# Optimization experiments

Measured on AMD Instinct MI355X. Metric: run time of the kernel, lower is better.

## Reference

```python
import jax, jax.numpy as jnp
from jax import lax
import numpy as np

H, W = 512, 1024
PAD = 7            # (kernel_size*2)//2 used for the 1x1 box-conv padding
POOL = 7           # max-pool NMS window
TOP_K = 200
NC = 34            # num semantic classes
B = 2
Hp, Wp = H + 2 * PAD, W + 2 * PAD


def _xy():
    # matches registered xy_coords buffer: (x,y) grids, 1-based
    xg = jnp.tile(jnp.arange(1, W + 1, dtype=jnp.float32)[None, :], (H, 1))
    yg = jnp.tile(jnp.arange(1, H + 1, dtype=jnp.float32)[:, None], (1, W))
    return jnp.stack([xg, yg], 0)  # [2,H,W]


def setup_inputs():
    key = jax.random.key(0)
    k1, k2 = jax.random.split(key)
    segmentation_probs = jax.random.normal(k1, (B, NC, H, W), jnp.float32)
    xy = _xy()
    blk = 64.0
    sx = jnp.floor((xy[0] - 1.0) / blk) * blk + blk / 2.0
    sy = jnp.floor((xy[1] - 1.0) / blk) * blk + blk / 2.0
    snapped = jnp.stack([sx, sy], 0)  # per-pixel block-center vote target
    noise = 0.05 * jax.random.normal(k2, (B, 2, H, W), jnp.float32)
    center_regressions = xy[None] - snapped[None] + noise
    center_maps_placeholder = jnp.zeros((1,), jnp.float32)
    return {"segmentation_probs": segmentation_probs,
            "center_maps_placeholder": center_maps_placeholder,
            "center_regressions": center_regressions}


def _assign(ccp, centers, valid):
    # ccp [B,2,H,W] predicted (x,y) centers per pixel; centers [B,K,2] as (y,x)
    # in padded coords (replicates original frame mismatch); valid [B,K].
    # Streaming argmin over K centers: O(B*H*W) memory.
    Bn = ccp.shape[0]
    def step(carry, k):
        bd, bi = carry
        cy = centers[:, k, 0].astype(jnp.float32)[:, None, None]
        cx = centers[:, k, 1].astype(jnp.float32)[:, None, None]
        d = (ccp[:, 0] - cx) ** 2 + (ccp[:, 1] - cy) ** 2  # sqrt omitted: argmin-invariant
        d = jnp.where(valid[:, k][:, None, None], d, jnp.inf)
        upd = d < bd
        return (jnp.where(upd, d, bd), jnp.where(upd, k, bi)), None
    init = (jnp.full((Bn, H, W), jnp.inf, jnp.float32),
            jnp.full((Bn, H, W), -1, jnp.int32))
    (bd, bi), _ = lax.scan(step, init, jnp.arange(TOP_K, dtype=jnp.int32))
    return bi + 1  # label 0 <=> no valid center


def _seg_sum(v, lab):
    return jax.ops.segment_sum(v.ravel(), lab.ravel(), num_segments=TOP_K + 1)

def _seg_min(v, lab):
    return jax.ops.segment_min(v.ravel(), lab.ravel(), num_segments=TOP_K + 1)

def _seg_max(v, lab):
    return jax.ops.segment_max(v.ravel(), lab.ravel(), num_segments=TOP_K + 1)


def _forward(segmentation_probs, center_regressions):
    seg_probs = jax.nn.softmax(segmentation_probs, axis=1)          # [B,NC,H,W]
    seg_map = jnp.argmax(segmentation_probs, axis=1).astype(jnp.float32)  # [B,H,W]
    xy = _xy()
    ccp = xy[None] - center_regressions                             # [B,2,H,W]
    # Threshold(23.99,50) then <=33  <=>  class in (23.99, 33]
    things = (seg_map > 23.99) & (seg_map <= 33.0)

    # ---- vote scatter (unique+counts == scatter-add of ones) ----
    vx = jnp.round(ccp[:, 0]).astype(jnp.int32)
    vy = jnp.round(ccp[:, 1]).astype(jnp.int32)
    ok = things & (vx >= 0) & (vy >= 0) & (vx < W) & (vy < H)
    flat = jnp.where(ok, vy * W + vx, H * W)                        # invalid -> dummy bin
    vote = jax.vmap(lambda ix: jnp.zeros(H * W + 1, jnp.float32).at[ix.ravel()].add(1.0))(flat)
    vote = vote[:, : H * W].reshape(-1, H, W)

    # ---- 1x1 box conv with padding=7 (just zero-pads), maxpool NMS ----
    aggr = jnp.pad(vote, ((0, 0), (PAD, PAD), (PAD, PAD)))          # [B,Hp,Wp]
    pooled = lax.reduce_window(aggr, -jnp.inf, lax.max, (1, POOL, POOL), (1, 1, 1),
                               [(0, 0), (POOL // 2, POOL // 2), (POOL // 2, POOL // 2)])
    nms = jnp.where(pooled == aggr, aggr, 0.0)
    cm = jnp.where(nms > 50.0, nms, 0.0)                            # Threshold(50,0)

    # ---- top-k centers by vote count ----
    vals = jnp.where(cm > 0.0, aggr, -1.0).reshape(-1, Hp * Wp)
    tv, ti = lax.top_k(vals, TOP_K)
    coords = jnp.stack([ti // Wp, ti % Wp], -1)                     # [B,K,2] (y,x)
    cvalid = tv > 0.0
    any_c = cvalid.any(-1)
    thingsi = things.astype(jnp.int32)

    lab0 = _assign(ccp, coords, cvalid) * thingsi
    lab0 = jnp.where(any_c[:, None, None], lab0, 0)

    ones_hw = jnp.ones((H, W), jnp.float32)
    ygrid = jnp.tile(jnp.arange(H, dtype=jnp.float32)[:, None], (1, W))
    xgrid = jnp.tile(jnp.arange(W, dtype=jnp.float32)[None, :], (H, 1))

    # ---- b_box_ratio_pruning2 ----
    cnt = jax.vmap(_seg_sum, (None, 0))(ones_hw, lab0)              # [B,K+1]
    ymin = jax.vmap(_seg_min, (None, 0))(ygrid, lab0)
    ymax = jax.vmap(_seg_max, (None, 0))(ygrid, lab0)
    xmin = jax.vmap(_seg_min, (None, 0))(xgrid, lab0)
    xmax = jax.vmap(_seg_max, (None, 0))(xgrid, lab0)
    ratio = cnt / ((ymax - ymin + 1.0) * (xmax - xmin + 1.0))
    g1 = ((cnt > 0) & (ratio > 0.3))[:, 1:]                         # [B,K] good slots
    n1 = g1.sum(-1)
    lab1s = _assign(ccp, coords, g1) * thingsi
    nl1 = jnp.cumsum(g1.astype(jnp.int32), -1)                      # compact relabel 1..n1
    lab1 = jax.vmap(lambda nl, l: jnp.where(l > 0, nl[l - 1], 0))(nl1, lab1s)
    lab1 = jnp.where((n1 > 0)[:, None, None], lab1, lab0)

    # ---- remove_high_mean_centers (indexes ORIGINAL sorted coords, as in source) ----
    cnt2 = jax.vmap(_seg_sum, (None, 0))(ones_hw, lab1)
    sx = jax.vmap(_seg_sum)(center_regressions[:, 0], lab1)
    sy = jax.vmap(_seg_sum)(center_regressions[:, 1], lab1)
    mx = sx / jnp.maximum(cnt2, 1.0)
    my = sy / jnp.maximum(cnt2, 1.0)
    g2 = ((cnt2 > 0) & (jnp.abs(mx) < 10.0) & (jnp.abs(my) < 10.0))[:, 1:]
    n2 = g2.sum(-1)
    lab2s = _assign(ccp, coords, g2) * thingsi
    nl2 = jnp.cumsum(g2.astype(jnp.int32), -1)
    lab2 = jax.vmap(lambda nl, l: jnp.where(l > 0, nl[l - 1], 0))(nl2, lab2s)
    final = jnp.where((n2 > 0)[:, None, None], lab2, lab1)

    # ---- separate_inst_maps: per-instance class (mode), mean class prob, size ----
    segc = seg_map.astype(jnp.int32)
    hidx = final * NC + segc
    hist = jax.vmap(lambda ix: jax.ops.segment_sum(
        jnp.ones(H * W, jnp.float32), ix.ravel(), num_segments=(TOP_K + 1) * NC))(hidx)
    hist = hist.reshape(-1, TOP_K + 1, NC)
    inst_class = jnp.argmax(hist, -1)                               # [B,K+1]
    # S[b,c,j] = sum of seg_probs[b,c] over pixels of instance j
    S = jax.vmap(lambda p, l: jax.vmap(lambda pc: _seg_sum(pc, l))(p))(seg_probs, final)
    cntf = jax.vmap(_seg_sum, (None, 0))(ones_hw, final)
    Sg = jnp.take_along_axis(jnp.swapaxes(S, 1, 2), inst_class[..., None], -1)[..., 0]
    seg_prob = Sg / jnp.maximum(cntf, 1.0)                          # [B,K+1]
    return final, seg_map, inst_class, seg_prob, cntf


def reference(segmentation_probs, center_maps_placeholder, center_regressions):
    return _forward(segmentation_probs, center_regressions)
```

## Files before the change

### kernel.cpp

```cpp
#include <hip/hip_runtime.h>
#include <stdint.h>

#define HH   512
#define WW   1024
#define BB   2
#define NCC  34
#define PADK 7
#define TOPK 200
#define NSEG (TOPK + 1)
#define WPAD (WW + 2 * PADK)
#define NPIX (HH * WW)
#define CAP  12288
#define INTMAXC  0x7FFFFFFF
#define INTMINC  (-0x7FFFFFFF - 1)

struct Prm {
  const float* seg; const float* cr;
  float* out_final; float* out_segmap; float* out_instc; float* out_prob; float* out_cntf;
  int32_t* labA; int32_t* labB; float* mbuf; float* invs; uint8_t* segc;
  int* ymin; int* ymax; int* xmin; int* xmax; int* instc;
  uint4* zero4; int nzero4;
  uint32_t* cand_cnt; uint32_t* cand_val; uint32_t* cand_idx;
  float* slotx; float* sloty; int* n0;
  float* l1x; float* l1y; int* n1;
  float* l2x; float* l2y; int* n2;
  uint32_t* cnt0; uint32_t* cnt2; long long* sxq; long long* syq;
  uint32_t* hist; long long* Ssel;
};

__global__ __launch_bounds__(256) void k_clear(Prm p) {
  int t = blockIdx.x * 256 + threadIdx.x;
  if (t < BB * NPIX / 4) reinterpret_cast<uint4*>(p.labA)[t] = make_uint4(0u, 0u, 0u, 0u);
  if (t < p.nzero4) p.zero4[t] = make_uint4(0u, 0u, 0u, 0u);
  if (t < BB * NSEG) {
    p.ymin[t] = INTMAXC; p.ymax[t] = INTMINC; p.xmin[t] = INTMAXC; p.xmax[t] = INTMINC;
  }
}

__global__ __launch_bounds__(256) void k_pixel(Prm p) {
  int t = blockIdx.x * 256 + threadIdx.x;
  int b = t >> 17;
  int pp = (t & 131071) << 2;
  int h = pp >> 10, w = pp & 1023;
  size_t i = (size_t)b * NPIX + pp;
  const float* base = p.seg + (size_t)b * NCC * NPIX + pp;
  float4 m = *reinterpret_cast<const float4*>(base);
  float4 s = make_float4(__expf(m.x), __expf(m.y), __expf(m.z), __expf(m.w));
  int4 am = make_int4(0, 0, 0, 0);
  #pragma unroll
  for (int c = 1; c < NCC; ++c) {
    float4 x = *reinterpret_cast<const float4*>(base + (size_t)c * NPIX);
    s.x += __expf(x.x); if (x.x > m.x) { m.x = x.x; am.x = c; }
    s.y += __expf(x.y); if (x.y > m.y) { m.y = x.y; am.y = c; }
    s.z += __expf(x.z); if (x.z > m.z) { m.z = x.z; am.z = c; }
    s.w += __expf(x.w); if (x.w > m.w) { m.w = x.w; am.w = c; }
  }
  *reinterpret_cast<float4*>(p.out_segmap + i) =
      make_float4((float)am.x, (float)am.y, (float)am.z, (float)am.w);
  *reinterpret_cast<uchar4*>(p.segc + i) =
      make_uchar4((unsigned char)am.x, (unsigned char)am.y, (unsigned char)am.z, (unsigned char)am.w);
  *reinterpret_cast<float4*>(p.mbuf + i) = m;
  *reinterpret_cast<float4*>(p.invs + i) =
      make_float4(__expf(m.x) / s.x, __expf(m.y) / s.y, __expf(m.z) / s.z, __expf(m.w) / s.w);

  const float* c0 = p.cr + (size_t)b * 2 * NPIX + pp;
  float4 r0 = *reinterpret_cast<const float4*>(c0);
  float4 r1 = *reinterpret_cast<const float4*>(c0 + NPIX);
  float crx[4] = {r0.x, r0.y, r0.z, r0.w};
  float cry[4] = {r1.x, r1.y, r1.z, r1.w};
  int amA[4] = {am.x, am.y, am.z, am.w};
  int tgt[4];
  #pragma unroll
  for (int q = 0; q < 4; ++q) {
    tgt[q] = -1;
    if (amA[q] >= 24) {
      float ccx = (float)(w + q + 1) - crx[q];
      float ccy = (float)(h + 1) - cry[q];
      float rx = rintf(ccx), ry = rintf(ccy);
      if (rx >= 0.f && ry >= 0.f && rx < (float)WW && ry < (float)HH)
        tgt[q] = (int)ry * WW + (int)rx;
    }
  }
  int lane = threadIdx.x & 63;
  uint32_t* vb = (uint32_t*)p.labA + (size_t)b * NPIX;
  #pragma unroll
  for (int q = 0; q < 4; ++q) {
    int tq = tgt[q];
    unsigned long long act = __ballot(tq >= 0);
    while (act) {
      int leader = __ffsll(act) - 1;
      int tl = __shfl(tq, leader);
      unsigned long long mt = __ballot(tq == tl);
      if (lane == leader) atomicAdd(&vb[tl], (uint32_t)__popcll(mt & act));
      act &= ~mt;
    }
  }
}

__global__ __launch_bounds__(256) void k_nms(Prm p) {
  int t = blockIdx.x * 256 + threadIdx.x;
  int b = t >> 17;
  int pp = (t & 131071) << 2;
  int h = pp >> 10, w0 = pp & 1023;
  const uint32_t* vb = (const uint32_t*)p.labA + (size_t)b * NPIX;
  uint4 v4 = *reinterpret_cast<const uint4*>(vb + pp);
  uint32_t vv[4] = {v4.x, v4.y, v4.z, v4.w};
  #pragma unroll
  for (int q = 0; q < 4; ++q) {
    uint32_t v = vv[q];
    if (v <= 50u) continue;
    int w = w0 + q;
    bool peak = true;
    for (int dy = -3; dy <= 3 && peak; ++dy) {
      int yy = h + dy; if (yy < 0 || yy >= HH) continue;
      for (int dx = -3; dx <= 3; ++dx) {
        int xx = w + dx; if (xx < 0 || xx >= WW) continue;
        if (vb[yy * WW + xx] > v) { peak = false; break; }
      }
    }
    if (!peak) continue;
    uint32_t pos = atomicAdd(&p.cand_cnt[b], 1u);
    if (pos < CAP) {
      p.cand_val[b * CAP + pos] = v;
      p.cand_idx[b * CAP + pos] = (uint32_t)((h + PADK) * WPAD + (w + PADK));
    }
  }
}

__global__ void k_topk(Prm p) {
  int b = blockIdx.x;
  int n = (int)p.cand_cnt[b]; if (n > CAP) n = CAP;
  const uint32_t* cv = p.cand_val + b * CAP;
  const uint32_t* ci = p.cand_idx + b * CAP;
  for (int i = threadIdx.x; i < n; i += blockDim.x) {
    unsigned long long ki = ((unsigned long long)cv[i] << 20) | (unsigned long long)(0xFFFFFu - ci[i]);
    int r = 0;
    for (int j = 0; j < n; ++j) {
      unsigned long long kj = ((unsigned long long)cv[j] << 20) | (unsigned long long)(0xFFFFFu - ci[j]);
      r += (kj > ki) ? 1 : 0;
    }
    if (r < TOPK) {
      uint32_t idx = ci[i];
      p.slotx[b * TOPK + r] = (float)(idx % WPAD);
      p.sloty[b * TOPK + r] = (float)(idx / WPAD);
    }
  }
  if (threadIdx.x == 0) p.n0[b] = (n < TOPK) ? n : TOPK;
}

__device__ __forceinline__ int prune_centers(int n, const float* __restrict__ sxs,
    const float* __restrict__ sys, float minx, float maxx, float miny, float maxy,
    short* __restrict__ clist, int lane) {
  #pragma unroll
  for (int o = 32; o; o >>= 1) {
    minx = fminf(minx, __shfl_xor(minx, o));
    maxx = fmaxf(maxx, __shfl_xor(maxx, o));
    miny = fminf(miny, __shfl_xor(miny, o));
    maxy = fmaxf(maxy, __shfl_xor(maxy, o));
  }
  float cx0 = 0.5f * (minx + maxx), rx = 0.5f * (maxx - minx) + 0.5f;
  float cy0 = 0.5f * (miny + maxy), ry = 0.5f * (maxy - miny) + 0.5f;
  float lo[4];
  float ub = 3.4e38f;
  #pragma unroll
  for (int c = 0; c < 4; ++c) {
    int k = c * 64 + lane;
    float l = 3.4e38f;
    if (k < n) {
      float dx = fabsf(sxs[k] - cx0), dy = fabsf(sys[k] - cy0);
      float hx = dx + rx, hy = dy + ry;
      ub = fminf(ub, hx * hx + hy * hy);
      float lx = fmaxf(dx - rx, 0.f), ly = fmaxf(dy - ry, 0.f);
      l = lx * lx + ly * ly;
    }
    lo[c] = l;
  }
  #pragma unroll
  for (int o = 32; o; o >>= 1) ub = fminf(ub, __shfl_xor(ub, o));
  ub += 1.0f;
  int m = 0;
  unsigned long long lmlt = (1ull << lane) - 1ull;
  #pragma unroll
  for (int c = 0; c < 4; ++c) {
    int k = c * 64 + lane;
    bool keep = (k < n) && (lo[c] <= ub);
    unsigned long long msk = __ballot(keep);
    if (keep) clist[m + (int)__popcll(msk & lmlt)] = (short)k;
    m += (int)__popcll(msk);
  }
  return m;
}

__device__ __forceinline__ void assign4_exact(int m, const short* __restrict__ clist,
    const float* __restrict__ sxs, const float* __restrict__ sys,
    const float* ccx, const float* ccy, const unsigned char* cls, int* l) {
  float bd[4] = {3.4e38f, 3.4e38f, 3.4e38f, 3.4e38f};
  int bk[4] = {0, 0, 0, 0};
  for (int j = 0; j < m; ++j) {
    int k = (int)clist[j];
    float cxk = sxs[k], cyk = sys[k];
    #pragma unroll
    for (int q = 0; q < 4; ++q) {
      float dx = ccx[q] - cxk, dy = ccy[q] - cyk;
      float d = __fadd_rn(__fmul_rn(dx, dx), __fmul_rn(dy, dy));
      if (d < bd[q]) { bd[q] = d; bk[q] = k; }
    }
  }
  #pragma unroll
  for (int q = 0; q < 4; ++q) l[q] = (cls[q] >= 24) ? bk[q] + 1 : 0;
}

__global__ __launch_bounds__(256) void k_assign0(Prm p) {
  int b = blockIdx.y, h = blockIdx.x;
  __shared__ float sxs[TOPK], sys[TOPK];
  __shared__ short clists[4][TOPK];
  __shared__ uint32_t sc[NSEG];
  __shared__ int sx0[NSEG], sx1[NSEG];
  int n = p.n0[b];
  for (int k = threadIdx.x; k < n; k += 256) { sxs[k] = p.slotx[b * TOPK + k]; sys[k] = p.sloty[b * TOPK + k]; }
  for (int j = threadIdx.x; j < NSEG; j += 256) { sc[j] = 0; sx0[j] = INTMAXC; sx1[j] = INTMINC; }
  __syncthreads();
  int w = threadIdx.x * 4;
  size_t i = (size_t)b * NPIX + h * WW + w;
  const float* c0 = p.cr + (size_t)b * 2 * NPIX + h * WW + w;
  uchar4 sc4 = *reinterpret_cast<const uchar4*>(p.segc + i);
  float4 r0 = *reinterpret_cast<const float4*>(c0);
  float4 r1 = *reinterpret_cast<const float4*>(c0 + NPIX);
  int l[4];
  if (n == 0) { l[0] = l[1] = l[2] = l[3] = 0; }
  else {
    float ccx[4], ccy[4];
    #pragma unroll
    for (int q = 0; q < 4; ++q) {
      ccx[q] = (float)(w + q + 1) - ((const float*)&r0)[q];
      ccy[q] = (float)(h + 1) - ((const float*)&r1)[q];
    }
    float mnx = fminf(fminf(ccx[0], ccx[1]), fminf(ccx[2], ccx[3]));
    float mxx = fmaxf(fmaxf(ccx[0], ccx[1]), fmaxf(ccx[2], ccx[3]));
    float mny = fminf(fminf(ccy[0], ccy[1]), fminf(ccy[2], ccy[3]));
    float mxy = fmaxf(fmaxf(ccy[0], ccy[1]), fmaxf(ccy[2], ccy[3]));
    int lane = threadIdx.x & 63, wv = threadIdx.x >> 6;
    int m = prune_centers(n, sxs, sys, mnx, mxx, mny, mxy, clists[wv], lane);
    unsigned char cls[4] = {sc4.x, sc4.y, sc4.z, sc4.w};
    assign4_exact(m, clists[wv], sxs, sys, ccx, ccy, cls, l);
  }
  *reinterpret_cast<int4*>(p.labA + i) = make_int4(l[0], l[1], l[2], l[3]);
  int cur = -1; uint32_t rc = 0; int rx0 = 0, rx1 = 0;
  #pragma unroll
  for (int q = 0; q < 4; ++q) {
    int lq = l[q], x = w + q;
    if (lq == cur) { rc++; rx1 = x; }
    else {
      if (cur > 0) { atomicAdd(&sc[cur], rc); atomicMin(&sx0[cur], rx0); atomicMax(&sx1[cur], rx1); }
      cur = lq; rc = 1; rx0 = rx1 = x;
    }
  }
  if (cur > 0) { atomicAdd(&sc[cur], rc); atomicMin(&sx0[cur], rx0); atomicMax(&sx1[cur], rx1); }
  __syncthreads();
  for (int j = threadIdx.x; j < NSEG; j += 256) {
    if (sc[j]) {
      atomicAdd(&p.cnt0[b * NSEG + j], sc[j]);
      atomicMin(&p.ymin[b * NSEG + j], h); atomicMax(&p.ymax[b * NSEG + j], h);
      atomicMin(&p.xmin[b * NSEG + j], sx0[j]); atomicMax(&p.xmax[b * NSEG + j], sx1[j]);
    }
  }
}

__global__ void k_build1(Prm p) {
  int b = blockIdx.x;
  __shared__ int good[TOPK], pref[TOPK];
  int k = threadIdx.x;
  if (k < TOPK) {
    uint32_t c = p.cnt0[b * NSEG + k + 1];
    int g = 0;
    if (c > 0) {
      int j = b * NSEG + k + 1;
      float area = (float)((p.ymax[j] - p.ymin[j] + 1) * (p.xmax[j] - p.xmin[j] + 1));
      float ratio = (float)c / area;
      g = (ratio > 0.3f) ? 1 : 0;
    }
    good[k] = g;
  }
  __syncthreads();
  if (threadIdx.x == 0) {
    int s = 0;
    for (int j = 0; j < TOPK; ++j) { pref[j] = s; s += good[j]; }
    p.n1[b] = s;
  }
  __syncthreads();
  if (k < TOPK && good[k]) {
    int r = pref[k];
    p.l1x[b * TOPK + r] = p.slotx[b * TOPK + k];
    p.l1y[b * TOPK + r] = p.sloty[b * TOPK + k];
  }
}

__global__ __launch_bounds__(256) void k_assign1(Prm p) {
  int b = blockIdx.y, h = blockIdx.x;
  __shared__ float sxs[TOPK], sys[TOPK];
  __shared__ short clists[4][TOPK];
  __shared__ uint32_t sc[NSEG];
  __shared__ unsigned long long ssx[NSEG], ssy[NSEG];
  int n = p.n1[b];
  for (int k = threadIdx.x; k < n; k += 256) { sxs[k] = p.l1x[b * TOPK + k]; sys[k] = p.l1y[b * TOPK + k]; }
  for (int j = threadIdx.x; j < NSEG; j += 256) { sc[j] = 0; ssx[j] = 0; ssy[j] = 0; }
  __syncthreads();
  int w = threadIdx.x * 4;
  size_t i = (size_t)b * NPIX + h * WW + w;
  const float* c0 = p.cr + (size_t)b * 2 * NPIX + h * WW + w;
  uchar4 sc4 = *reinterpret_cast<const uchar4*>(p.segc + i);
  float4 r0 = *reinterpret_cast<const float4*>(c0);
  float4 r1 = *reinterpret_cast<const float4*>(c0 + NPIX);
  int l[4];
  if (n == 0) { int4 f = *reinterpret_cast<const int4*>(p.labA + i); l[0]=f.x; l[1]=f.y; l[2]=f.z; l[3]=f.w; }
  else {
    float ccx[4], ccy[4];
    #pragma unroll
    for (int q = 0; q < 4; ++q) {
      ccx[q] = (float)(w + q + 1) - ((const float*)&r0)[q];
      ccy[q] = (float)(h + 1) - ((const float*)&r1)[q];
    }
    float mnx = fminf(fminf(ccx[0], ccx[1]), fminf(ccx[2], ccx[3]));
    float mxx = fmaxf(fmaxf(ccx[0], ccx[1]), fmaxf(ccx[2], ccx[3]));
    float mny = fminf(fminf(ccy[0], ccy[1]), fminf(ccy[2], ccy[3]));
    float mxy = fmaxf(fmaxf(ccy[0], ccy[1]), fmaxf(ccy[2], ccy[3]));
    int lane = threadIdx.x & 63, wv = threadIdx.x >> 6;
    int m = prune_centers(n, sxs, sys, mnx, mxx, mny, mxy, clists[wv], lane);
    unsigned char cls[4] = {sc4.x, sc4.y, sc4.z, sc4.w};
    assign4_exact(m, clists[wv], sxs, sys, ccx, ccy, cls, l);
  }
  *reinterpret_cast<int4*>(p.labB + i) = make_int4(l[0], l[1], l[2], l[3]);
  float crx[4] = {r0.x, r0.y, r0.z, r0.w};
  float cry[4] = {r1.x, r1.y, r1.z, r1.w};
  int cur = -1; uint32_t rc = 0; long long ax = 0, ay = 0;
  #pragma unroll
  for (int q = 0; q < 4; ++q) {
    int lq = l[q];
    long long qx = __double2ll_rn((double)crx[q] * 1048576.0);
    long long qy = __double2ll_rn((double)cry[q] * 1048576.0);
    if (lq == cur) { rc++; ax += qx; ay += qy; }
    else {
      if (cur > 0) { atomicAdd(&sc[cur], rc);
                     atomicAdd(&ssx[cur], (unsigned long long)ax);
                     atomicAdd(&ssy[cur], (unsigned long long)ay); }
      cur = lq; rc = 1; ax = qx; ay = qy;
    }
  }
  if (cur > 0) { atomicAdd(&sc[cur], rc);
                 atomicAdd(&ssx[cur], (unsigned long long)ax);
                 atomicAdd(&ssy[cur], (unsigned long long)ay); }
  __syncthreads();
  for (int j = threadIdx.x; j < NSEG; j += 256) {
    if (sc[j]) {
      atomicAdd(&p.cnt2[b * NSEG + j], sc[j]);
      atomicAdd((unsigned long long*)&p.sxq[b * NSEG + j], ssx[j]);
      atomicAdd((unsigned long long*)&p.syq[b * NSEG + j], ssy[j]);
    }
  }
}

__global__ void k_build2(Prm p) {
  int b = blockIdx.x;
  __shared__ int good[TOPK], pref[TOPK];
  int k = threadIdx.x;
  if (k < TOPK) {
    uint32_t c = p.cnt2[b * NSEG + k + 1];
    int g = 0;
    if (c > 0) {
      double inv = 1.0 / (double)c;
      double mx = ((double)p.sxq[b * NSEG + k + 1] * (1.0 / 1048576.0)) * inv;
      double my = ((double)p.syq[b * NSEG + k + 1] * (1.0 / 1048576.0)) * inv;
      g = (fabs(mx) < 10.0 && fabs(my) < 10.0) ? 1 : 0;
    }
    good[k] = g;
  }
  __syncthreads();
  if (threadIdx.x == 0) {
    int s = 0;
    for (int j = 0; j < TOPK; ++j) { pref[j] = s; s += good[j]; }
    p.n2[b] = s;
  }
  __syncthreads();
  if (k < TOPK && good[k]) {
    int r = pref[k];
    p.l2x[b * TOPK + r] = p.slotx[b * TOPK + k];
    p.l2y[b * TOPK + r] = p.sloty[b * TOPK + k];
  }
}

__global__ __launch_bounds__(256) void k_assign2(Prm p) {
  int b = blockIdx.y, h = blockIdx.x;
  __shared__ float sxs[TOPK], sys[TOPK];
  __shared__ short clists[4][TOPK];
  __shared__ uint32_t sh[NSEG * NCC];
  int n = p.n2[b];
  for (int k = threadIdx.x; k < n; k += 256) { sxs[k] = p.l2x[b * TOPK + k]; sys[k] = p.l2y[b * TOPK + k]; }
  for (int j = threadIdx.x; j < NSEG * NCC; j += 256) sh[j] = 0;
  __syncthreads();
  int w = threadIdx.x * 4;
  size_t i = (size_t)b * NPIX + h * WW + w;
  const float* c0 = p.cr + (size_t)b * 2 * NPIX + h * WW + w;
  uchar4 sc4 = *reinterpret_cast<const uchar4*>(p.segc + i);
  float4 r0 = *reinterpret_cast<const float4*>(c0);
  float4 r1 = *reinterpret_cast<const float4*>(c0 + NPIX);
  int l[4];
  if (n == 0) { int4 f = *reinterpret_cast<const int4*>(p.labB + i); l[0]=f.x; l[1]=f.y; l[2]=f.z; l[3]=f.w; }
  else {
    float ccx[4], ccy[4];
    #pragma unroll
    for (int q = 0; q < 4; ++q) {
      ccx[q] = (float)(w + q + 1) - ((const float*)&r0)[q];
      ccy[q] = (float)(h + 1) - ((const float*)&r1)[q];
    }
    float mnx = fminf(fminf(ccx[0], ccx[1]), fminf(ccx[2], ccx[3]));
    float mxx = fmaxf(fmaxf(ccx[0], ccx[1]), fmaxf(ccx[2], ccx[3]));
    float mny = fminf(fminf(ccy[0], ccy[1]), fminf(ccy[2], ccy[3]));
    float mxy = fmaxf(fmaxf(ccy[0], ccy[1]), fmaxf(ccy[2], ccy[3]));
    int lane = threadIdx.x & 63, wv = threadIdx.x >> 6;
    int m = prune_centers(n, sxs, sys, mnx, mxx, mny, mxy, clists[wv], lane);
    unsigned char cls[4] = {sc4.x, sc4.y, sc4.z, sc4.w};
    assign4_exact(m, clists[wv], sxs, sys, ccx, ccy, cls, l);
  }
  *reinterpret_cast<int4*>(p.labA + i) = make_int4(l[0], l[1], l[2], l[3]);
  *reinterpret_cast<float4*>(p.out_final + i) =
      make_float4((float)l[0], (float)l[1], (float)l[2], (float)l[3]);
  unsigned char cls[4] = {sc4.x, sc4.y, sc4.z, sc4.w};
  int curk = -1; uint32_t rc = 0;
  #pragma unroll
  for (int q = 0; q < 4; ++q) {
    int key = l[q] * NCC + (int)cls[q];
    if (key == curk) { rc++; }
    else { if (curk >= 0) atomicAdd(&sh[curk], rc); curk = key; rc = 1; }
  }
  if (curk >= 0) atomicAdd(&sh[curk], rc);
  __syncthreads();
  for (int j = threadIdx.x; j < NSEG * NCC; j += 256)
    if (sh[j]) atomicAdd(&p.hist[(size_t)b * NSEG * NCC + j], sh[j]);
}

__global__ void k_mode(Prm p) {
  int b = blockIdx.x;
  int j = threadIdx.x;
  if (j >= NSEG) return;
  const uint32_t* hr = p.hist + ((size_t)b * NSEG + j) * NCC;
  uint32_t bv = hr[0], s = hr[0]; int bc = 0;
  #pragma unroll
  for (int c = 1; c < NCC; ++c) {
    uint32_t v = hr[c]; s += v;
    if (v > bv) { bv = v; bc = c; }
  }
  p.instc[b * NSEG + j] = bc;
  p.out_instc[b * NSEG + j] = (float)bc;
  p.out_cntf[b * NSEG + j] = (float)s;
}

__global__ __launch_bounds__(256) void k_sg(Prm p) {
  int b = blockIdx.y;
  __shared__ unsigned long long ss[NSEG];
  __shared__ int icS[NSEG];
  for (int j = threadIdx.x; j < NSEG; j += 256) { ss[j] = 0; icS[j] = p.instc[b * NSEG + j]; }
  __syncthreads();
  int pp = (blockIdx.x * 256 + threadIdx.x) * 4;
  size_t i = (size_t)b * NPIX + pp;
  int4 l4 = *reinterpret_cast<const int4*>(p.labA + i);
  float4 mb = *reinterpret_cast<const float4*>(p.mbuf + i);
  float4 iv = *reinterpret_cast<const float4*>(p.invs + i);
  const float* sb = p.seg + (size_t)b * NCC * NPIX + pp;
  int lA[4] = {l4.x, l4.y, l4.z, l4.w};
  float mbA[4] = {mb.x, mb.y, mb.z, mb.w};
  float ivA[4] = {iv.x, iv.y, iv.z, iv.w};
  int cur = -1; long long acc = 0;
  #pragma unroll
  for (int q = 0; q < 4; ++q) {
    int lq = lA[q];
    int c = icS[lq];
    float x = sb[(size_t)c * NPIX + q];
    float pr = __expf(x - mbA[q]) * ivA[q];
    long long qv = __double2ll_rn((double)pr * 4294967296.0);
    if (lq == cur) acc += qv;
    else { if (cur >= 0) atomicAdd(&ss[cur], (unsigned long long)acc); cur = lq; acc = qv; }
  }
  if (cur >= 0) atomicAdd(&ss[cur], (unsigned long long)acc);
  __syncthreads();
  for (int j = threadIdx.x; j < NSEG; j += 256)
    if (ss[j]) atomicAdd((unsigned long long*)&p.Ssel[b * NSEG + j], ss[j]);
}

__global__ void k_prob(Prm p) {
  int i = blockIdx.x * blockDim.x + threadIdx.x;
  if (i >= BB * NSEG) return;
  double s = (double)p.Ssel[i] * (1.0 / 4294967296.0);
  float c = p.out_cntf[i];
  p.out_prob[i] = (float)(s / (double)fmaxf(c, 1.0f));
}

extern "C" void kernel_launch(void* const* d_in, const int* in_sizes, int n_in,
                              void* d_out, int out_size, void* d_ws, size_t ws_size,
                              hipStream_t stream) {
  float* out = (float*)d_out;
  Prm p;
  p.seg = (const float*)d_in[0];
  p.cr  = (const float*)d_in[2];
  p.out_final  = out;
  p.out_segmap = out + (size_t)BB * NPIX;
  p.out_instc  = out + (size_t)2 * BB * NPIX;
  p.out_prob   = p.out_instc + BB * NSEG;
  p.out_cntf   = p.out_prob + BB * NSEG;

  char* ws = (char*)d_ws;
  size_t off = 0;
  auto take = [&](size_t n) { size_t o = off; off += (n + 255) & ~(size_t)255; return o; };

  p.labA = (int32_t*)(ws + take((size_t)BB * NPIX * 4));
  p.labB = (int32_t*)(ws + take((size_t)BB * NPIX * 4));
  p.mbuf = (float*)(ws + take((size_t)BB * NPIX * 4));
  p.invs = (float*)(ws + take((size_t)BB * NPIX * 4));
  p.segc = (uint8_t*)(ws + take((size_t)BB * NPIX));
  p.ymin = (int*)(ws + take(BB * NSEG * 4));
  p.ymax = (int*)(ws + take(BB * NSEG * 4));
  p.xmin = (int*)(ws + take(BB * NSEG * 4));
  p.xmax = (int*)(ws + take(BB * NSEG * 4));

  size_t zero_begin = off;
  p.cand_cnt = (uint32_t*)(ws + take(BB * 4));
  p.cand_val = (uint32_t*)(ws + take((size_t)BB * CAP * 4));
  p.cand_idx = (uint32_t*)(ws + take((size_t)BB * CAP * 4));
  p.slotx = (float*)(ws + take(BB * TOPK * 4));
  p.sloty = (float*)(ws + take(BB * TOPK * 4));
  p.n0 = (int*)(ws + take(BB * 4));
  p.l1x = (float*)(ws + take(BB * TOPK * 4));
  p.l1y = (float*)(ws + take(BB * TOPK * 4));
  p.n1 = (int*)(ws + take(BB * 4));
  p.l2x = (float*)(ws + take(BB * TOPK * 4));
  p.l2y = (float*)(ws + take(BB * TOPK * 4));
  p.n2 = (int*)(ws + take(BB * 4));
  p.cnt0 = (uint32_t*)(ws + take(BB * NSEG * 4));
  p.cnt2 = (uint32_t*)(ws + take(BB * NSEG * 4));
  p.sxq = (long long*)(ws + take(BB * NSEG * 8));
  p.syq = (long long*)(ws + take(BB * NSEG * 8));
  p.hist = (uint32_t*)(ws + take((size_t)BB * NSEG * NCC * 4));
  p.instc = (int*)(ws + take(BB * NSEG * 4));
  p.Ssel = (long long*)(ws + take(BB * NSEG * 8));
  size_t zero_end = off;

  if (ws_size < off) return;

  p.zero4 = (uint4*)(ws + zero_begin);
  p.nzero4 = (int)((zero_end - zero_begin) / 16);

  k_clear<<<BB * NPIX / 4 / 256, 256, 0, stream>>>(p);
  k_pixel<<<BB * NPIX / 4 / 256, 256, 0, stream>>>(p);
  k_nms<<<BB * NPIX / 4 / 256, 256, 0, stream>>>(p);
  k_topk<<<BB, 256, 0, stream>>>(p);
  dim3 rgrid(HH, BB);
  k_assign0<<<rgrid, 256, 0, stream>>>(p);
  k_build1<<<BB, 256, 0, stream>>>(p);
  k_assign1<<<rgrid, 256, 0, stream>>>(p);
  k_build2<<<BB, 256, 0, stream>>>(p);
  k_assign2<<<rgrid, 256, 0, stream>>>(p);
  k_mode<<<BB, 256, 0, stream>>>(p);
  k_sg<<<dim3(NPIX / 1024, BB), 256, 0, stream>>>(p);
  k_prob<<<(BB * NSEG + 255) / 256, 256, 0, stream>>>(p);
}
```

Baseline: 134.2 us.

## Fuse top-k, build and mode kernels into per-row assign blocks

```diff
diff --git a/kernel.cpp b/kernel.cpp
--- a/kernel.cpp
+++ b/kernel.cpp
@@ -11,19 +11,17 @@
 #define WPAD (WW + 2 * PADK)
 #define NPIX (HH * WW)
 #define CAP  12288
+#define KSTG 1024
 #define INTMAXC  0x7FFFFFFF
 #define INTMINC  (-0x7FFFFFFF - 1)
 
 struct Prm {
   const float* seg; const float* cr;
   float* out_final; float* out_segmap; float* out_instc; float* out_prob; float* out_cntf;
-  int32_t* labA; int32_t* labB; float* mbuf; float* invs; uint8_t* segc;
-  int* ymin; int* ymax; int* xmin; int* xmax; int* instc;
+  int32_t* labA; int32_t* labB; float* pinv; uint8_t* segc;
+  int* ymin; int* ymax; int* xmin; int* xmax;
   uint4* zero4; int nzero4;
   uint32_t* cand_cnt; uint32_t* cand_val; uint32_t* cand_idx;
-  float* slotx; float* sloty; int* n0;
-  float* l1x; float* l1y; int* n1;
-  float* l2x; float* l2y; int* n2;
   uint32_t* cnt0; uint32_t* cnt2; long long* sxq; long long* syq;
   uint32_t* hist; long long* Ssel;
 };
@@ -59,9 +57,8 @@
       make_float4((float)am.x, (float)am.y, (float)am.z, (float)am.w);
   *reinterpret_cast<uchar4*>(p.segc + i) =
       make_uchar4((unsigned char)am.x, (unsigned char)am.y, (unsigned char)am.z, (unsigned char)am.w);
-  *reinterpret_cast<float4*>(p.mbuf + i) = m;
-  *reinterpret_cast<float4*>(p.invs + i) =
-      make_float4(__expf(m.x) / s.x, __expf(m.y) / s.y, __expf(m.z) / s.z, __expf(m.w) / s.w);
+  *reinterpret_cast<float4*>(p.pinv + i) =
+      make_float4(1.f / s.x, 1.f / s.y, 1.f / s.z, 1.f / s.w);
 
   const float* c0 = p.cr + (size_t)b * 2 * NPIX + pp;
   float4 r0 = *reinterpret_cast<const float4*>(c0);
@@ -127,25 +124,52 @@
   }
 }
 
-__global__ void k_topk(Prm p) {
-  int b = blockIdx.x;
+__device__ __forceinline__ int block_topk(const Prm& p, int b,
+    unsigned long long* keysS, float* osx, float* osy) {
   int n = (int)p.cand_cnt[b]; if (n > CAP) n = CAP;
   const uint32_t* cv = p.cand_val + b * CAP;
   const uint32_t* ci = p.cand_idx + b * CAP;
-  for (int i = threadIdx.x; i < n; i += blockDim.x) {
+  bool stg = (n <= KSTG);
+  if (stg)
+    for (int j = threadIdx.x; j < n; j += 256)
+      keysS[j] = ((unsigned long long)cv[j] << 20) | (unsigned long long)(0xFFFFFu - ci[j]);
+  __syncthreads();
+  for (int i = threadIdx.x; i < n; i += 256) {
     unsigned long long ki = ((unsigned long long)cv[i] << 20) | (unsigned long long)(0xFFFFFu - ci[i]);
     int r = 0;
-    for (int j = 0; j < n; ++j) {
-      unsigned long long kj = ((unsigned long long)cv[j] << 20) | (unsigned long long)(0xFFFFFu - ci[j]);
-      r += (kj > ki) ? 1 : 0;
+    if (stg) { for (int j = 0; j < n; ++j) r += (keysS[j] > ki) ? 1 : 0; }
+    else {
+      for (int j = 0; j < n; ++j) {
+        unsigned long long kj = ((unsigned long long)cv[j] << 20) | (unsigned long long)(0xFFFFFu - ci[j]);
+        r += (kj > ki) ? 1 : 0;
+      }
     }
     if (r < TOPK) {
       uint32_t idx = ci[i];
-      p.slotx[b * TOPK + r] = (float)(idx % WPAD);
-      p.sloty[b * TOPK + r] = (float)(idx / WPAD);
-    }
-  }
-  if (threadIdx.x == 0) p.n0[b] = (n < TOPK) ? n : TOPK;
+      osx[r] = (float)(idx % WPAD);
+      osy[r] = (float)(idx / WPAD);
+    }
+  }
+  __syncthreads();
+  return (n < TOPK) ? n : TOPK;
+}
+
+__device__ __forceinline__ int block_compact(int good, const float* osx, const float* osy,
+    float* dxs, float* dys, int* wsumS) {
+  int lane = threadIdx.x & 63, wv = threadIdx.x >> 6;
+  unsigned long long mask = __ballot(good);
+  if (lane == 0) wsumS[wv] = (int)__popcll(mask);
+  __syncthreads();
+  int off = 0;
+  #pragma unroll
+  for (int t = 0; t < 4; ++t) off += (t < wv) ? wsumS[t] : 0;
+  int total = wsumS[0] + wsumS[1] + wsumS[2] + wsumS[3];
+  if (good) {
+    int pos = off + (int)__popcll(mask & ((1ull << lane) - 1ull));
+    dxs[pos] = osx[threadIdx.x]; dys[pos] = osy[threadIdx.x];
+  }
+  __syncthreads();
+  return total;
 }
 
 __device__ __forceinline__ int prune_centers(int n, const float* __restrict__ sxs,
@@ -210,16 +234,35 @@
   for (int q = 0; q < 4; ++q) l[q] = (cls[q] >= 24) ? bk[q] + 1 : 0;
 }
 
+__device__ __forceinline__ void assign_body(const Prm& p, int b, int h, int n,
+    const float* sxs, const float* sys, short* clist_wv,
+    const uchar4 sc4, const float4 r0, const float4 r1, int* l) {
+  int w = threadIdx.x * 4;
+  float ccx[4], ccy[4];
+  #pragma unroll
+  for (int q = 0; q < 4; ++q) {
+    ccx[q] = (float)(w + q + 1) - ((const float*)&r0)[q];
+    ccy[q] = (float)(h + 1) - ((const float*)&r1)[q];
+  }
+  float mnx = fminf(fminf(ccx[0], ccx[1]), fminf(ccx[2], ccx[3]));
+  float mxx = fmaxf(fmaxf(ccx[0], ccx[1]), fmaxf(ccx[2], ccx[3]));
+  float mny = fminf(fminf(ccy[0], ccy[1]), fminf(ccy[2], ccy[3]));
+  float mxy = fmaxf(fmaxf(ccy[0], ccy[1]), fmaxf(ccy[2], ccy[3]));
+  int lane = threadIdx.x & 63;
+  int m = prune_centers(n, sxs, sys, mnx, mxx, mny, mxy, clist_wv, lane);
+  unsigned char cls[4] = {sc4.x, sc4.y, sc4.z, sc4.w};
+  assign4_exact(m, clist_wv, sxs, sys, ccx, ccy, cls, l);
+}
+
 __global__ __launch_bounds__(256) void k_assign0(Prm p) {
   int b = blockIdx.y, h = blockIdx.x;
   __shared__ float sxs[TOPK], sys[TOPK];
   __shared__ short clists[4][TOPK];
   __shared__ uint32_t sc[NSEG];
   __shared__ int sx0[NSEG], sx1[NSEG];
-  int n = p.n0[b];
-  for (int k = threadIdx.x; k < n; k += 256) { sxs[k] = p.slotx[b * TOPK + k]; sys[k] = p.sloty[b * TOPK + k]; }
+  __shared__ unsigned long long keysS[KSTG];
   for (int j = threadIdx.x; j < NSEG; j += 256) { sc[j] = 0; sx0[j] = INTMAXC; sx1[j] = INTMINC; }
-  __syncthreads();
+  int n = block_topk(p, b, keysS, sxs, sys);
   int w = threadIdx.x * 4;
   size_t i = (size_t)b * NPIX + h * WW + w;
   const float* c0 = p.cr + (size_t)b * 2 * NPIX + h * WW + w;
@@ -228,22 +271,7 @@
   float4 r1 = *reinterpret_cast<const float4*>(c0 + NPIX);
   int l[4];
   if (n == 0) { l[0] = l[1] = l[2] = l[3] = 0; }
-  else {
-    float ccx[4], ccy[4];
-    #pragma unroll
-    for (int q = 0; q < 4; ++q) {
-      ccx[q] = (float)(w + q + 1) - ((const float*)&r0)[q];
-      ccy[q] = (float)(h + 1) - ((const float*)&r1)[q];
-    }
-    float mnx = fminf(fminf(ccx[0], ccx[1]), fminf(ccx[2], ccx[3]));
-    float mxx = fmaxf(fmaxf(ccx[0], ccx[1]), fmaxf(ccx[2], ccx[3]));
-    float mny = fminf(fminf(ccy[0], ccy[1]), fminf(ccy[2], ccy[3]));
-    float mxy = fmaxf(fmaxf(ccy[0], ccy[1]), fmaxf(ccy[2], ccy[3]));
-    int lane = threadIdx.x & 63, wv = threadIdx.x >> 6;
-    int m = prune_centers(n, sxs, sys, mnx, mxx, mny, mxy, clists[wv], lane);
-    unsigned char cls[4] = {sc4.x, sc4.y, sc4.z, sc4.w};
-    assign4_exact(m, clists[wv], sxs, sys, ccx, ccy, cls, l);
-  }
+  else assign_body(p, b, h, n, sxs, sys, clists[threadIdx.x >> 6], sc4, r0, r1, l);
   *reinterpret_cast<int4*>(p.labA + i) = make_int4(l[0], l[1], l[2], l[3]);
   int cur = -1; uint32_t rc = 0; int rx0 = 0, rx1 = 0;
   #pragma unroll
@@ -266,45 +294,29 @@
   }
 }
 
-__global__ void k_build1(Prm p) {
-  int b = blockIdx.x;
-  __shared__ int good[TOPK], pref[TOPK];
+__global__ __launch_bounds__(256) void k_assign1(Prm p) {
+  int b = blockIdx.y, h = blockIdx.x;
+  __shared__ float osx[TOPK], osy[TOPK];
+  __shared__ float sxs[TOPK], sys[TOPK];
+  __shared__ short clists[4][TOPK];
+  __shared__ uint32_t sc[NSEG];
+  __shared__ unsigned long long ssx[NSEG], ssy[NSEG];
+  __shared__ unsigned long long keysS[KSTG];
+  __shared__ int wsumS[4];
+  for (int j = threadIdx.x; j < NSEG; j += 256) { sc[j] = 0; ssx[j] = 0; ssy[j] = 0; }
+  block_topk(p, b, keysS, osx, osy);
   int k = threadIdx.x;
+  int good = 0;
   if (k < TOPK) {
     uint32_t c = p.cnt0[b * NSEG + k + 1];
-    int g = 0;
     if (c > 0) {
       int j = b * NSEG + k + 1;
       float area = (float)((p.ymax[j] - p.ymin[j] + 1) * (p.xmax[j] - p.xmin[j] + 1));
       float ratio = (float)c / area;
-      g = (ratio > 0.3f) ? 1 : 0;
-    }
-    good[k] = g;
-  }
-  __syncthreads();
-  if (threadIdx.x == 0) {
-    int s = 0;
-    for (int j = 0; j < TOPK; ++j) { pref[j] = s; s += good[j]; }
-    p.n1[b] = s;
-  }
-  __syncthreads();
-  if (k < TOPK && good[k]) {
-    int r = pref[k];
-    p.l1x[b * TOPK + r] = p.slotx[b * TOPK + k];
-    p.l1y[b * TOPK + r] = p.sloty[b * TOPK + k];
-  }
-}
-
-__global__ __launch_bounds__(256) void k_assign1(Prm p) {
-  int b = blockIdx.y, h = blockIdx.x;
-  __shared__ float sxs[TOPK], sys[TOPK];
-  __shared__ short clists[4][TOPK];
-  __shared__ uint32_t sc[NSEG];
-  __shared__ unsigned long long ssx[NSEG], ssy[NSEG];
-  int n = p.n1[b];
-  for (int k = threadIdx.x; k < n; k += 256) { sxs[k] = p.l1x[b * TOPK + k]; sys[k] = p.l1y[b * TOPK + k]; }
-  for (int j = threadIdx.x; j < NSEG; j += 256) { sc[j] = 0; ssx[j] = 0; ssy[j] = 0; }
-  __syncthreads();
+      good = (ratio > 0.3f) ? 1 : 0;
+    }
+  }
+  int n = block_compact(good, osx, osy, sxs, sys, wsumS);
   int w = threadIdx.x * 4;
   size_t i = (size_t)b * NPIX + h * WW + w;
   const float* c0 = p.cr + (size_t)b * 2 * NPIX + h * WW + w;
@@ -313,22 +325,7 @@
   float4 r1 = *reinterpret_cast<const float4*>(c0 + NPIX);
   int l[4];
   if (n == 0) { int4 f = *reinterpret_cast<const int4*>(p.labA + i); l[0]=f.x; l[1]=f.y; l[2]=f.z; l[3]=f.w; }
-  else {
-    float ccx[4], ccy[4];
-    #pragma unroll
-    for (int q = 0; q < 4; ++q) {
-      ccx[q] = (float)(w + q + 1) - ((const float*)&r0)[q];
-      ccy[q] = (float)(h + 1) - ((const float*)&r1)[q];
-    }
-    float mnx = fminf(fminf(ccx[0], ccx[1]), fminf(ccx[2], ccx[3]));
-    float mxx = fmaxf(fmaxf(ccx[0], ccx[1]), fmaxf(ccx[2], ccx[3]));
-    float mny = fminf(fminf(ccy[0], ccy[1]), fminf(ccy[2], ccy[3]));
-    float mxy = fmaxf(fmaxf(ccy[0], ccy[1]), fmaxf(ccy[2], ccy[3]));
-    int lane = threadIdx.x & 63, wv = threadIdx.x >> 6;
-    int m = prune_centers(n, sxs, sys, mnx, mxx, mny, mxy, clists[wv], lane);
-    unsigned char cls[4] = {sc4.x, sc4.y, sc4.z, sc4.w};
-    assign4_exact(m, clists[wv], sxs, sys, ccx, ccy, cls, l);
-  }
+  else assign_body(p, b, h, n, sxs, sys, clists[threadIdx.x >> 6], sc4, r0, r1, l);
   *reinterpret_cast<int4*>(p.labB + i) = make_int4(l[0], l[1], l[2], l[3]);
   float crx[4] = {r0.x, r0.y, r0.z, r0.w};
   float cry[4] = {r1.x, r1.y, r1.z, r1.w};
@@ -359,44 +356,28 @@
   }
 }
 
-__global__ void k_build2(Prm p) {
-  int b = blockIdx.x;
-  __shared__ int good[TOPK], pref[TOPK];
+__global__ __launch_bounds__(256) void k_assign2(Prm p) {
+  int b = blockIdx.y, h = blockIdx.x;
+  __shared__ float osx[TOPK], osy[TOPK];
+  __shared__ float sxs[TOPK], sys[TOPK];
+  __shared__ short clists[4][TOPK];
+  __shared__ uint32_t sh[NSEG * NCC];
+  __shared__ unsigned long long keysS[KSTG];
+  __shared__ int wsumS[4];
+  for (int j = threadIdx.x; j < NSEG * NCC; j += 256) sh[j] = 0;
+  block_topk(p, b, keysS, osx, osy);
   int k = threadIdx.x;
+  int good = 0;
   if (k < TOPK) {
     uint32_t c = p.cnt2[b * NSEG + k + 1];
-    int g = 0;
     if (c > 0) {
       double inv = 1.0 / (double)c;
       double mx = ((double)p.sxq[b * NSEG + k + 1] * (1.0 / 1048576.0)) * inv;
       double my = ((double)p.syq[b * NSEG + k + 1] * (1.0 / 1048576.0)) * inv;
-      g = (fabs(mx) < 10.0 && fabs(my) < 10.0) ? 1 : 0;
-    }
-    good[k] = g;
-  }
-  __syncthreads();
-  if (threadIdx.x == 0) {
-    int s = 0;
-    for (int j = 0; j < TOPK; ++j) { pref[j] = s; s += good[j]; }
-    p.n2[b] = s;
-  }
-  __syncthreads();
-  if (k < TOPK && good[k]) {
-    int r = pref[k];
-    p.l2x[b * TOPK + r] = p.slotx[b * TOPK + k];
-    p.l2y[b * TOPK + r] = p.sloty[b * TOPK + k];
-  }
-}
-
-__global__ __launch_bounds__(256) void k_assign2(Prm p) {
-  int b = blockIdx.y, h = blockIdx.x;
-  __shared__ float sxs[TOPK], sys[TOPK];
-  __shared__ short clists[4][TOPK];
-  __shared__ uint32_t sh[NSEG * NCC];
-  int n = p.n2[b];
-  for (int k = threadIdx.x; k < n; k += 256) { sxs[k] = p.l2x[b * TOPK + k]; sys[k] = p.l2y[b * TOPK + k]; }
-  for (int j = threadIdx.x; j < NSEG * NCC; j += 256) sh[j] = 0;
-  __syncthreads();
+      good = (fabs(mx) < 10.0 && fabs(my) < 10.0) ? 1 : 0;
+    }
+  }
+  int n = block_compact(good, osx, osy, sxs, sys, wsumS);
   int w = threadIdx.x * 4;
   size_t i = (size_t)b * NPIX + h * WW + w;
   const float* c0 = p.cr + (size_t)b * 2 * NPIX + h * WW + w;
@@ -405,22 +386,7 @@
   float4 r1 = *reinterpret_cast<const float4*>(c0 + NPIX);
   int l[4];
   if (n == 0) { int4 f = *reinterpret_cast<const int4*>(p.labB + i); l[0]=f.x; l[1]=f.y; l[2]=f.z; l[3]=f.w; }
-  else {
-    float ccx[4], ccy[4];
-    #pragma unroll
-    for (int q = 0; q < 4; ++q) {
-      ccx[q] = (float)(w + q + 1) - ((const float*)&r0)[q];
-      ccy[q] = (float)(h + 1) - ((const float*)&r1)[q];
-    }
-    float mnx = fminf(fminf(ccx[0], ccx[1]), fminf(ccx[2], ccx[3]));
-    float mxx = fmaxf(fmaxf(ccx[0], ccx[1]), fmaxf(ccx[2], ccx[3]));
-    float mny = fminf(fminf(ccy[0], ccy[1]), fminf(ccy[2], ccy[3]));
-    float mxy = fmaxf(fmaxf(ccy[0], ccy[1]), fmaxf(ccy[2], ccy[3]));
-    int lane = threadIdx.x & 63, wv = threadIdx.x >> 6;
-    int m = prune_centers(n, sxs, sys, mnx, mxx, mny, mxy, clists[wv], lane);
-    unsigned char cls[4] = {sc4.x, sc4.y, sc4.z, sc4.w};
-    assign4_exact(m, clists[wv], sxs, sys, ccx, ccy, cls, l);
-  }
+  else assign_body(p, b, h, n, sxs, sys, clists[threadIdx.x >> 6], sc4, r0, r1, l);
   *reinterpret_cast<int4*>(p.labA + i) = make_int4(l[0], l[1], l[2], l[3]);
   *reinterpret_cast<float4*>(p.out_final + i) =
       make_float4((float)l[0], (float)l[1], (float)l[2], (float)l[3]);
@@ -438,36 +404,32 @@
     if (sh[j]) atomicAdd(&p.hist[(size_t)b * NSEG * NCC + j], sh[j]);
 }
 
-__global__ void k_mode(Prm p) {
-  int b = blockIdx.x;
-  int j = threadIdx.x;
-  if (j >= NSEG) return;
-  const uint32_t* hr = p.hist + ((size_t)b * NSEG + j) * NCC;
-  uint32_t bv = hr[0], s = hr[0]; int bc = 0;
-  #pragma unroll
-  for (int c = 1; c < NCC; ++c) {
-    uint32_t v = hr[c]; s += v;
-    if (v > bv) { bv = v; bc = c; }
-  }
-  p.instc[b * NSEG + j] = bc;
-  p.out_instc[b * NSEG + j] = (float)bc;
-  p.out_cntf[b * NSEG + j] = (float)s;
-}
-
 __global__ __launch_bounds__(256) void k_sg(Prm p) {
   int b = blockIdx.y;
   __shared__ unsigned long long ss[NSEG];
   __shared__ int icS[NSEG];
-  for (int j = threadIdx.x; j < NSEG; j += 256) { ss[j] = 0; icS[j] = p.instc[b * NSEG + j]; }
+  for (int j = threadIdx.x; j < NSEG; j += 256) {
+    const uint32_t* hr = p.hist + ((size_t)b * NSEG + j) * NCC;
+    uint32_t bv = hr[0], ssum = hr[0]; int bc = 0;
+    #pragma unroll
+    for (int c = 1; c < NCC; ++c) {
+      uint32_t v = hr[c]; ssum += v;
+      if (v > bv) { bv = v; bc = c; }
+    }
+    icS[j] = bc;
+    ss[j] = 0;
+    if (blockIdx.x == 0) {
+      p.out_instc[b * NSEG + j] = (float)bc;
+      p.out_cntf[b * NSEG + j] = (float)ssum;
+    }
+  }
   __syncthreads();
   int pp = (blockIdx.x * 256 + threadIdx.x) * 4;
   size_t i = (size_t)b * NPIX + pp;
   int4 l4 = *reinterpret_cast<const int4*>(p.labA + i);
-  float4 mb = *reinterpret_cast<const float4*>(p.mbuf + i);
-  float4 iv = *reinterpret_cast<const float4*>(p.invs + i);
+  float4 iv = *reinterpret_cast<const float4*>(p.pinv + i);
   const float* sb = p.seg + (size_t)b * NCC * NPIX + pp;
   int lA[4] = {l4.x, l4.y, l4.z, l4.w};
-  float mbA[4] = {mb.x, mb.y, mb.z, mb.w};
   float ivA[4] = {iv.x, iv.y, iv.z, iv.w};
   int cur = -1; long long acc = 0;
   #pragma unroll
@@ -475,7 +437,7 @@
     int lq = lA[q];
     int c = icS[lq];
     float x = sb[(size_t)c * NPIX + q];
-    float pr = __expf(x - mbA[q]) * ivA[q];
+    float pr = __expf(x) * ivA[q];
     long long qv = __double2ll_rn((double)pr * 4294967296.0);
     if (lq == cur) acc += qv;
     else { if (cur >= 0) atomicAdd(&ss[cur], (unsigned long long)acc); cur = lq; acc = qv; }
@@ -513,8 +475,7 @@
 
   p.labA = (int32_t*)(ws + take((size_t)BB * NPIX * 4));
   p.labB = (int32_t*)(ws + take((size_t)BB * NPIX * 4));
-  p.mbuf = (float*)(ws + take((size_t)BB * NPIX * 4));
-  p.invs = (float*)(ws + take((size_t)BB * NPIX * 4));
+  p.pinv = (float*)(ws + take((size_t)BB * NPIX * 4));
   p.segc = (uint8_t*)(ws + take((size_t)BB * NPIX));
   p.ymin = (int*)(ws + take(BB * NSEG * 4));
   p.ymax = (int*)(ws + take(BB * NSEG * 4));
@@ -525,21 +486,11 @@
   p.cand_cnt = (uint32_t*)(ws + take(BB * 4));
   p.cand_val = (uint32_t*)(ws + take((size_t)BB * CAP * 4));
   p.cand_idx = (uint32_t*)(ws + take((size_t)BB * CAP * 4));
-  p.slotx = (float*)(ws + take(BB * TOPK * 4));
-  p.sloty = (float*)(ws + take(BB * TOPK * 4));
-  p.n0 = (int*)(ws + take(BB * 4));
-  p.l1x = (float*)(ws + take(BB * TOPK * 4));
-  p.l1y = (float*)(ws + take(BB * TOPK * 4));
-  p.n1 = (int*)(ws + take(BB * 4));
-  p.l2x = (float*)(ws + take(BB * TOPK * 4));
-  p.l2y = (float*)(ws + take(BB * TOPK * 4));
-  p.n2 = (int*)(ws + take(BB * 4));
   p.cnt0 = (uint32_t*)(ws + take(BB * NSEG * 4));
   p.cnt2 = (uint32_t*)(ws + take(BB * NSEG * 4));
   p.sxq = (long long*)(ws + take(BB * NSEG * 8));
   p.syq = (long long*)(ws + take(BB * NSEG * 8));
   p.hist = (uint32_t*)(ws + take((size_t)BB * NSEG * NCC * 4));
-  p.instc = (int*)(ws + take(BB * NSEG * 4));
   p.Ssel = (long long*)(ws + take(BB * NSEG * 8));
   size_t zero_end = off;
 
@@ -551,14 +502,10 @@
   k_clear<<<BB * NPIX / 4 / 256, 256, 0, stream>>>(p);
   k_pixel<<<BB * NPIX / 4 / 256, 256, 0, stream>>>(p);
   k_nms<<<BB * NPIX / 4 / 256, 256, 0, stream>>>(p);
-  k_topk<<<BB, 256, 0, stream>>>(p);
   dim3 rgrid(HH, BB);
   k_assign0<<<rgrid, 256, 0, stream>>>(p);
-  k_build1<<<BB, 256, 0, stream>>>(p);
   k_assign1<<<rgrid, 256, 0, stream>>>(p);
-  k_build2<<<BB, 256, 0, stream>>>(p);
   k_assign2<<<rgrid, 256, 0, stream>>>(p);
-  k_mode<<<BB, 256, 0, stream>>>(p);
   k_sg<<<dim3(NPIX / 1024, BB), 256, 0, stream>>>(p);
   k_prob<<<(BB * NSEG + 255) / 256, 256, 0, stream>>>(p);
 }
```

New measurement: 127.3 us. -5.2%, faster.
